# Kernel optimization log

Hardware: AMD Instinct MI355X
Metric: run time of the kernel (lower is better)

The kernel has to match this reference:

```python
import jax, jax.numpy as jnp
import numpy as np


def setup_inputs() -> dict:
    key = jax.random.key(0)
    ks = jax.random.split(key, 9)
    B, C, H, W = 8, 256, 64, 64
    Co = 256
    s = 1.0 / np.sqrt(C)
    return {
        "x": jax.random.normal(ks[0], (B, C, H, W), dtype=jnp.float32),
        "wq": jax.random.normal(ks[1], (Co, C), dtype=jnp.float32) * s,
        "bq": jnp.zeros((Co,), dtype=jnp.float32),
        "wk": jax.random.normal(ks[2], (Co, C), dtype=jnp.float32) * s,
        "bk": jnp.zeros((Co,), dtype=jnp.float32),
        "wv": jax.random.normal(ks[3], (Co, C), dtype=jnp.float32) * s,
        "bv": jnp.zeros((Co,), dtype=jnp.float32),
        "wo": jax.random.normal(ks[4], (C, Co), dtype=jnp.float32) * s,
        "bo": jnp.zeros((C,), dtype=jnp.float32),
    }


def reference(x, wq, bq, wk, bk, wv, bv, wo, bo):
    B, C, H, W = x.shape
    # 1x1 conv == per-pixel matmul. Flatten spatial dims: [B, N, C], N = H*W
    xf = x.reshape(B, C, H * W).transpose(0, 2, 1)  # [B, N, C]
    q = jnp.einsum("bnc,oc->bno", xf, wq) + bq      # [B, N, Co]
    k = jnp.einsum("bnc,oc->bno", xf, wk) + bk      # [B, N, Co]
    v = jnp.einsum("bnc,oc->bno", xf, wv) + bv      # [B, N, Co]
    # attention[b, i, j] = q[b, i] . k[b, j]  (no scaling, matches source)
    attn = jax.nn.softmax(jnp.einsum("bio,bjo->bij", q, k), axis=-1)  # [B, N, N]
    # out[b, i, c] = sum_j attn[b, i, j] * v[b, j, c]
    out = jnp.einsum("bij,bjo->bio", attn, v)       # [B, N, Co]
    out = jnp.einsum("bno,co->bnc", out, wo) + bo   # [B, N, C]
    return out.transpose(0, 2, 1).reshape(B, C, H, W)
```

## Files before the change

kernel.cpp:

```cpp
#include <hip/hip_runtime.h>
#include <hip/hip_fp16.h>

typedef _Float16 f16;
typedef _Float16 f16x4 __attribute__((ext_vector_type(4)));
typedef _Float16 f16x8 __attribute__((ext_vector_type(8)));
typedef float f32x4 __attribute__((ext_vector_type(4)));
typedef float f32x16 __attribute__((ext_vector_type(16)));
typedef unsigned int u32;
typedef u32 u32x4 __attribute__((ext_vector_type(4)));

static constexpr int CB = 8;
static constexpr int CC = 256;
static constexpr int CN = 4096;

#define MFMA(a, b, c)   __builtin_amdgcn_mfma_f32_16x16x32_f16((a), (b), (c), 0, 0, 0)
#define MFMA32(a, b, c) __builtin_amdgcn_mfma_f32_32x32x16_f16((a), (b), (c), 0, 0, 0)

__device__ __forceinline__ void gll16(const void* g, void* l) {
  __builtin_amdgcn_global_load_lds(
      (const __attribute__((address_space(1))) unsigned int*)g,
      (__attribute__((address_space(3))) unsigned int*)l, 16, 0, 0);
}

__device__ __forceinline__ void plswap(u32& a, u32& b) {
  asm volatile("v_permlane32_swap_b32 %0, %1" : "+v"(a), "+v"(b));
}

__device__ __forceinline__ u32 pk(float lo, float hi) {
  auto h = __builtin_amdgcn_cvt_pkrtz(lo, hi);
  return __builtin_bit_cast(u32, h);
}

__global__ __launch_bounds__(256) void prep_weights(const float* __restrict__ wq,
    const float* __restrict__ wk, const float* __restrict__ wv,
    const float* __restrict__ wo, f16* __restrict__ W) {
  int i = blockIdx.x * 256 + threadIdx.x;
  W[i]          = (f16)wq[i];
  W[65536 + i]  = (f16)wk[i];
  W[131072 + i] = (f16)wv[i];
  W[196608 + i] = (f16)wo[i];
}

__global__ __launch_bounds__(256) void qkv_kernel(const float* __restrict__ x,
    const f16* __restrict__ Wq, const f16* __restrict__ Wk, const f16* __restrict__ Wv,
    const float* __restrict__ bq, const float* __restrict__ bk, const float* __restrict__ bv,
    f16* __restrict__ Q, f16* __restrict__ K, f16* __restrict__ Vt) {
  __shared__ f16 xf[64][264];
  const int b  = blockIdx.x >> 6;
  const int n0 = (blockIdx.x & 63) << 6;
  const int t  = threadIdx.x;
  const float* xb = x + (size_t)b * CC * CN;
  {
    int c = t >> 4;
    const int nn = (t & 15) << 2;
    #pragma unroll
    for (int pass = 0; pass < 16; ++pass, c += 16) {
      const float4 v = *(const float4*)(xb + (size_t)c * CN + n0 + nn);
      xf[nn + 0][c] = (f16)v.x;
      xf[nn + 1][c] = (f16)v.y;
      xf[nn + 2][c] = (f16)v.z;
      xf[nn + 3][c] = (f16)v.w;
    }
  }
  __syncthreads();
  const int w = t >> 6, l = t & 63, lr = l & 15, lh = l >> 4;

  f16x8 xff[8];
  #pragma unroll
  for (int kk = 0; kk < 8; ++kk)
    xff[kk] = *(const f16x8*)&xf[w * 16 + lr][kk * 32 + lh * 8];

  const size_t qkrow = ((size_t)b * CN + n0 + w * 16 + lr) * CC;

  #pragma unroll 1
  for (int mat = 0; mat < 2; ++mat) {
    const f16* W = mat ? Wk : Wq;
    const float* bias = mat ? bk : bq;
    f16* dst = mat ? K : Q;
    f32x4 acc[16];
    #pragma unroll
    for (int m = 0; m < 16; ++m) acc[m] = f32x4{0.f, 0.f, 0.f, 0.f};
    #pragma unroll
    for (int kk = 0; kk < 8; ++kk) {
      #pragma unroll
      for (int m = 0; m < 16; ++m) {
        f16x8 af = *(const f16x8*)&W[(size_t)(m * 16 + lr) * CC + kk * 32 + lh * 8];
        acc[m] = MFMA(af, xff[kk], acc[m]);
      }
    }
    #pragma unroll
    for (int m = 0; m < 16; ++m) {
      const int o = m * 16 + lh * 4;
      const float4 bs = *(const float4*)&bias[o];
      f16x4 hv;
      hv[0] = (f16)(acc[m][0] + bs.x);
      hv[1] = (f16)(acc[m][1] + bs.y);
      hv[2] = (f16)(acc[m][2] + bs.z);
      hv[3] = (f16)(acc[m][3] + bs.w);
      *(f16x4*)&dst[qkrow + o] = hv;
    }
  }
  {
    f32x4 acc[16];
    #pragma unroll
    for (int m = 0; m < 16; ++m) acc[m] = f32x4{0.f, 0.f, 0.f, 0.f};
    #pragma unroll
    for (int kk = 0; kk < 8; ++kk) {
      #pragma unroll
      for (int m = 0; m < 16; ++m) {
        f16x8 bf = *(const f16x8*)&Wv[(size_t)(m * 16 + lr) * CC + kk * 32 + lh * 8];
        acc[m] = MFMA(xff[kk], bf, acc[m]);
      }
    }
    #pragma unroll
    for (int m = 0; m < 16; ++m) {
      const int o = m * 16 + lr;
      const float bvs = bv[o];
      f16x4 hv;
      #pragma unroll
      for (int j = 0; j < 4; ++j) hv[j] = (f16)(acc[m][j] + bvs);
      *(f16x4*)&Vt[((size_t)b * CC + o) * CN + n0 + w * 16 + lh * 4] = hv;
    }
  }
}

__global__ __launch_bounds__(256, 2) void attn_kernel(const f16* __restrict__ Q,
    const f16* __restrict__ K, const f16* __restrict__ Vt,
    const f16* __restrict__ Wo, const float* __restrict__ bo,
    float* __restrict__ out) {
  __shared__ __align__(16) char SMEM[75264];

  const int bid = blockIdx.x;
  const int lb = ((bid & 7) << 6) | (bid >> 3);
  const int b  = lb >> 6;
  const int q0 = (lb & 63) << 6;
  const int par = (bid >> 3) & 1;
  const int tid = threadIdx.x;
  const int w  = tid >> 6, l = tid & 63, ln = l & 31, lh = l >> 5;
  const int g  = w >> 1, hv = w & 1;

  const f16* Qb = Q  + (size_t)b * CN * CC;
  const f16* Kb = K  + (size_t)b * CN * CC;
  const f16* Vb = Vt + (size_t)b * CC * CN;

  auto kfrm = [&](int buf, int ks) -> char* { return SMEM + (buf << 14) + (ks << 10); };
  auto vfrm = [&](int buf, int f)  -> char* { return SMEM + 32768 + (buf << 14) + (f << 10); };
  auto pfrm = [&](int pb, int fr)  -> char* { return SMEM + 65536 + (pb << 12) + (g << 11) + (fr << 10); };
  float* const MLm = (float*)(SMEM + 73728 + g * 256);
  float* const MLl = MLm + 32;
  auto AFa = [&](int pb) -> float* { return (float*)(SMEM + 74240 + (pb << 9) + (g << 8)); };

  auto stageK = [&](int buf, int kv0) {
    const f16* ksrc = Kb + (size_t)(kv0 + ln) * CC + (w * 4) * 16 + 8 * lh;
    #pragma unroll
    for (int j = 0; j < 4; ++j)
      gll16(ksrc + j * 16, kfrm(buf, w * 4 + j));
  };
  auto stageV = [&](int buf, int kv0) {
    #pragma unroll
    for (int p = 0; p < 2; ++p) {
      const int f = w * 4 + 2 * p;
      const f16* vsrc = Vb + (size_t)((f >> 1) * 32 + ln) * CN + kv0 + 8 * lh;
      gll16(vsrc,      vfrm(buf, f));
      gll16(vsrc + 16, vfrm(buf, f + 1));
    }
  };

  const int qrow = q0 + 32 * g + ln;
  f16x8 qf[16];
  #pragma unroll
  for (int ks = 0; ks < 16; ++ks)
    qf[ks] = *(const f16x8*)(Qb + (size_t)qrow * CC + ks * 16 + 8 * lh);

  f32x16 oacc[4];
  #pragma unroll
  for (int ot = 0; ot < 4; ++ot)
    #pragma unroll
    for (int i = 0; i < 16; ++i) oacc[ot][i] = 0.0f;

  auto pvstep = [&](int pb) {
    const float* af = AFa(pb);
    const float flag = af[32];
    if (flag != 0.0f) {
      #pragma unroll
      for (int r = 0; r < 16; ++r) {
        const float fr = af[(r & 3) + 8 * (r >> 2) + 4 * lh];
        #pragma unroll
        for (int ot = 0; ot < 4; ++ot) oacc[ot][r] *= fr;
      }
    }
    const f16x8 pa0 = *(const f16x8*)(pfrm(pb, 0) + l * 16);
    const f16x8 pa1 = *(const f16x8*)(pfrm(pb, 1) + l * 16);
    __builtin_amdgcn_s_setprio(1);
    #pragma unroll
    for (int ot = 0; ot < 4; ++ot) {
      const int f0 = 8 * hv + 2 * ot;
      const f16x8 v0 = *(const f16x8*)(vfrm(pb, f0) + l * 16);
      oacc[ot] = MFMA32(pa0, v0, oacc[ot]);
      const f16x8 v1 = *(const f16x8*)(vfrm(pb, f0 + 1) + l * 16);
      oacc[ot] = MFMA32(pa1, v1, oacc[ot]);
    }
    __builtin_amdgcn_s_setprio(0);
  };

  stageK(0, 0);
  __syncthreads();

  #pragma unroll 1
  for (int it = 0; it < 128; ++it) {
    const int cur = it & 1, prv = cur ^ 1;
    if (it < 127) stageK(prv, (it + 1) * 32);
    stageV(cur, it * 32);

    const bool own = (hv == ((it + par) & 1));

    f32x16 s;
    if (own) {
      f32x16 sa, sb;
      #pragma unroll
      for (int i = 0; i < 16; ++i) { sa[i] = 0.0f; sb[i] = 0.0f; }
      __builtin_amdgcn_s_setprio(1);
      #pragma unroll
      for (int ks = 0; ks < 8; ++ks) {
        const f16x8 kf0 = *(const f16x8*)(kfrm(cur, ks) + l * 16);
        sa = MFMA32(kf0, qf[ks], sa);
        const f16x8 kf1 = *(const f16x8*)(kfrm(cur, ks + 8) + l * 16);
        sb = MFMA32(kf1, qf[ks + 8], sb);
      }
      __builtin_amdgcn_s_setprio(0);
      #pragma unroll
      for (int i = 0; i < 16; ++i) s[i] = sa[i] + sb[i];
    }

    if (it > 0) pvstep(prv);

    if (own) {
      const float mprev = it ? MLm[ln] : -3e38f;
      const float lprev = it ? MLl[ln] : 0.0f;
      float mx8[8], mx4[4];
      #pragma unroll
      for (int i = 0; i < 8; ++i) mx8[i] = fmaxf(s[2 * i], s[2 * i + 1]);
      #pragma unroll
      for (int i = 0; i < 4; ++i) mx4[i] = fmaxf(mx8[2 * i], mx8[2 * i + 1]);
      float pmax = fmaxf(fmaxf(mx4[0], mx4[1]), fmaxf(mx4[2], mx4[3]));
      pmax = fmaxf(pmax, __shfl_xor(pmax, 32));
      const bool need = !__all(pmax - mprev <= 8.0f);
      const float mnew = need ? fmaxf(mprev, pmax) : mprev;
      float p[16];
      #pragma unroll
      for (int r = 0; r < 16; ++r) p[r] = __expf(s[r] - mnew);
      float sm8[8], sm4[4];
      #pragma unroll
      for (int i = 0; i < 8; ++i) sm8[i] = p[2 * i] + p[2 * i + 1];
      #pragma unroll
      for (int i = 0; i < 4; ++i) sm4[i] = sm8[2 * i] + sm8[2 * i + 1];
      float psum = (sm4[0] + sm4[1]) + (sm4[2] + sm4[3]);
      psum += __shfl_xor(psum, 32);
      float alpha = 1.0f, lnew;
      if (need) { alpha = __expf(mprev - mnew); lnew = lprev * alpha + psum; }
      else      { lnew = lprev + psum; }
      if (l < 32) {
        MLm[ln] = mnew;
        MLl[ln] = lnew;
        float* af = AFa(cur);
        af[ln] = alpha;
        if (ln == 0) af[32] = need ? 1.0f : 0.0f;
      }
      u32 pw[8];
      #pragma unroll
      for (int i = 0; i < 8; ++i) pw[i] = pk(p[2 * i], p[2 * i + 1]);
      plswap(pw[0], pw[2]); plswap(pw[1], pw[3]);
      plswap(pw[4], pw[6]); plswap(pw[5], pw[7]);
      *(u32x4*)(pfrm(cur, 0) + l * 16) = u32x4{pw[0], pw[1], pw[2], pw[3]};
      *(u32x4*)(pfrm(cur, 1) + l * 16) = u32x4{pw[4], pw[5], pw[6], pw[7]};
    }
    __syncthreads();
  }

  pvstep(1);
  float invv[16];
  #pragma unroll
  for (int r = 0; r < 16; ++r)
    invv[r] = 1.0f / MLl[(r & 3) + 8 * (r >> 2) + 4 * lh];
  __syncthreads();

  f16* const OT = (f16*)SMEM;
  #pragma unroll
  for (int r = 0; r < 16; ++r) {
    const int q = (r & 3) + 8 * (r >> 2) + 4 * lh;
    const int qq = 32 * g + q;
    #pragma unroll
    for (int ot = 0; ot < 4; ++ot)
      OT[qq * 264 + 128 * hv + ot * 32 + ln] = (f16)(oacc[ot][r] * invv[r]);
  }
  __syncthreads();

  {
    const int lr = l & 15, lq = l >> 4;
    const f16* orow = OT + (w * 16 + lr) * 264;
    f32x4 acc[16];
    #pragma unroll
    for (int m = 0; m < 16; ++m) acc[m] = f32x4{0.f, 0.f, 0.f, 0.f};
    #pragma unroll
    for (int kk = 0; kk < 8; ++kk) {
      const f16x8 bf = *(const f16x8*)&orow[kk * 32 + lq * 8];
      #pragma unroll
      for (int m = 0; m < 16; ++m) {
        f16x8 af = *(const f16x8*)&Wo[(size_t)(m * 16 + lr) * CC + kk * 32 + lq * 8];
        acc[m] = MFMA(af, bf, acc[m]);
      }
    }
    #pragma unroll
    for (int m = 0; m < 16; ++m) {
      const int c = m * 16 + lq * 4;
      const float4 bv4 = *(const float4*)&bo[c];
      const size_t base = ((size_t)b * CC + c) * CN + q0 + w * 16 + lr;
      out[base + 0 * (size_t)CN] = acc[m][0] + bv4.x;
      out[base + 1 * (size_t)CN] = acc[m][1] + bv4.y;
      out[base + 2 * (size_t)CN] = acc[m][2] + bv4.z;
      out[base + 3 * (size_t)CN] = acc[m][3] + bv4.w;
    }
  }
}

extern "C" void kernel_launch(void* const* d_in, const int* in_sizes, int n_in,
                              void* d_out, int out_size, void* d_ws, size_t ws_size,
                              hipStream_t stream) {
  const float* x  = (const float*)d_in[0];
  const float* wq = (const float*)d_in[1];
  const float* bq = (const float*)d_in[2];
  const float* wk = (const float*)d_in[3];
  const float* bk = (const float*)d_in[4];
  const float* wv = (const float*)d_in[5];
  const float* bv = (const float*)d_in[6];
  const float* wo = (const float*)d_in[7];
  const float* bo = (const float*)d_in[8];

  f16* W  = (f16*)d_ws;
  f16* Qd = W + 262144;
  f16* Kd = Qd + (size_t)CB * CN * CC;
  f16* Vt = Kd + (size_t)CB * CN * CC;

  prep_weights<<<256, 256, 0, stream>>>(wq, wk, wv, wo, W);
  qkv_kernel<<<512, 256, 0, stream>>>(x, W, W + 65536, W + 131072, bq, bk, bv, Qd, Kd, Vt);
  attn_kernel<<<512, 256, 0, stream>>>(Qd, Kd, Vt, W + 196608, bo, (float*)d_out);
}
```

Measured before the change: 378.2 us.

## Switch QKV projection to 32x32 MFMA tiles with 2 waves per block

Restructures the QKV projection kernel to use 128-thread blocks where each wave handles 32 pixels with 32x32x16 MFMAs instead of 16x16x32, processing two 32-wide output tiles at a time. Each weight fragment loaded from global memory now feeds a larger MFMA, cutting weight-load traffic per unit of work and the total instruction count. In exchange there are fewer waves per block (less latency hiding during the x staging loads), more registers are held in the x fragment array, and each thread does twice as many staging passes.

```diff
diff --git a/kernel.cpp b/kernel.cpp
--- a/kernel.cpp
+++ b/kernel.cpp
@@ -41,7 +41,7 @@
   W[196608 + i] = (f16)wo[i];
 }
 
-__global__ __launch_bounds__(256) void qkv_kernel(const float* __restrict__ x,
+__global__ __launch_bounds__(128) void qkv_kernel(const float* __restrict__ x,
     const f16* __restrict__ Wq, const f16* __restrict__ Wk, const f16* __restrict__ Wv,
     const float* __restrict__ bq, const float* __restrict__ bk, const float* __restrict__ bv,
     f16* __restrict__ Q, f16* __restrict__ K, f16* __restrict__ Vt) {
@@ -54,7 +54,7 @@
     int c = t >> 4;
     const int nn = (t & 15) << 2;
     #pragma unroll
-    for (int pass = 0; pass < 16; ++pass, c += 16) {
+    for (int pass = 0; pass < 32; ++pass, c += 8) {
       const float4 v = *(const float4*)(xb + (size_t)c * CN + n0 + nn);
       xf[nn + 0][c] = (f16)v.x;
       xf[nn + 1][c] = (f16)v.y;
@@ -63,63 +63,79 @@
     }
   }
   __syncthreads();
-  const int w = t >> 6, l = t & 63, lr = l & 15, lh = l >> 4;
-
-  f16x8 xff[8];
-  #pragma unroll
-  for (int kk = 0; kk < 8; ++kk)
-    xff[kk] = *(const f16x8*)&xf[w * 16 + lr][kk * 32 + lh * 8];
-
-  const size_t qkrow = ((size_t)b * CN + n0 + w * 16 + lr) * CC;
+  const int w = t >> 6, l = t & 63, ln = l & 31, lh = l >> 5;
+
+  f16x8 xff[16];
+  #pragma unroll
+  for (int kt = 0; kt < 16; ++kt)
+    xff[kt] = *(const f16x8*)&xf[w * 32 + ln][kt * 16 + lh * 8];
+
+  const size_t qkrow = ((size_t)b * CN + n0 + w * 32 + ln) * CC;
 
   #pragma unroll 1
   for (int mat = 0; mat < 2; ++mat) {
     const f16* W = mat ? Wk : Wq;
     const float* bias = mat ? bk : bq;
     f16* dst = mat ? K : Q;
-    f32x4 acc[16];
-    #pragma unroll
-    for (int m = 0; m < 16; ++m) acc[m] = f32x4{0.f, 0.f, 0.f, 0.f};
-    #pragma unroll
-    for (int kk = 0; kk < 8; ++kk) {
-      #pragma unroll
-      for (int m = 0; m < 16; ++m) {
-        f16x8 af = *(const f16x8*)&W[(size_t)(m * 16 + lr) * CC + kk * 32 + lh * 8];
-        acc[m] = MFMA(af, xff[kk], acc[m]);
-      }
-    }
-    #pragma unroll
-    for (int m = 0; m < 16; ++m) {
-      const int o = m * 16 + lh * 4;
-      const float4 bs = *(const float4*)&bias[o];
-      f16x4 hv;
-      hv[0] = (f16)(acc[m][0] + bs.x);
-      hv[1] = (f16)(acc[m][1] + bs.y);
-      hv[2] = (f16)(acc[m][2] + bs.z);
-      hv[3] = (f16)(acc[m][3] + bs.w);
-      *(f16x4*)&dst[qkrow + o] = hv;
-    }
-  }
-  {
-    f32x4 acc[16];
-    #pragma unroll
-    for (int m = 0; m < 16; ++m) acc[m] = f32x4{0.f, 0.f, 0.f, 0.f};
-    #pragma unroll
-    for (int kk = 0; kk < 8; ++kk) {
-      #pragma unroll
-      for (int m = 0; m < 16; ++m) {
-        f16x8 bf = *(const f16x8*)&Wv[(size_t)(m * 16 + lr) * CC + kk * 32 + lh * 8];
-        acc[m] = MFMA(xff[kk], bf, acc[m]);
-      }
-    }
-    #pragma unroll
-    for (int m = 0; m < 16; ++m) {
-      const int o = m * 16 + lr;
-      const float bvs = bv[o];
-      f16x4 hv;
-      #pragma unroll
-      for (int j = 0; j < 4; ++j) hv[j] = (f16)(acc[m][j] + bvs);
-      *(f16x4*)&Vt[((size_t)b * CC + o) * CN + n0 + w * 16 + lh * 4] = hv;
+    #pragma unroll 1
+    for (int ot = 0; ot < 8; ot += 2) {
+      f32x16 a0, a1;
+      #pragma unroll
+      for (int i = 0; i < 16; ++i) { a0[i] = 0.0f; a1[i] = 0.0f; }
+      #pragma unroll
+      for (int kt = 0; kt < 16; ++kt) {
+        const f16x8 af0 = *(const f16x8*)&W[(size_t)(ot * 32 + ln) * CC + kt * 16 + lh * 8];
+        a0 = MFMA32(af0, xff[kt], a0);
+        const f16x8 af1 = *(const f16x8*)&W[(size_t)(ot * 32 + 32 + ln) * CC + kt * 16 + lh * 8];
+        a1 = MFMA32(af1, xff[kt], a1);
+      }
+      #pragma unroll
+      for (int rg = 0; rg < 4; ++rg) {
+        const int o = ot * 32 + rg * 8 + lh * 4;
+        const float4 b0 = *(const float4*)&bias[o];
+        const float4 b1 = *(const float4*)&bias[o + 32];
+        f16x4 h0, h1;
+        h0[0] = (f16)(a0[rg * 4 + 0] + b0.x);
+        h0[1] = (f16)(a0[rg * 4 + 1] + b0.y);
+        h0[2] = (f16)(a0[rg * 4 + 2] + b0.z);
+        h0[3] = (f16)(a0[rg * 4 + 3] + b0.w);
+        h1[0] = (f16)(a1[rg * 4 + 0] + b1.x);
+        h1[1] = (f16)(a1[rg * 4 + 1] + b1.y);
+        h1[2] = (f16)(a1[rg * 4 + 2] + b1.z);
+        h1[3] = (f16)(a1[rg * 4 + 3] + b1.w);
+        *(f16x4*)&dst[qkrow + o]      = h0;
+        *(f16x4*)&dst[qkrow + o + 32] = h1;
+      }
+    }
+  }
+
+  #pragma unroll 1
+  for (int ot = 0; ot < 8; ot += 2) {
+    f32x16 a0, a1;
+    #pragma unroll
+    for (int i = 0; i < 16; ++i) { a0[i] = 0.0f; a1[i] = 0.0f; }
+    #pragma unroll
+    for (int kt = 0; kt < 16; ++kt) {
+      const f16x8 wf0 = *(const f16x8*)&Wv[(size_t)(ot * 32 + ln) * CC + kt * 16 + lh * 8];
+      a0 = MFMA32(xff[kt], wf0, a0);
+      const f16x8 wf1 = *(const f16x8*)&Wv[(size_t)(ot * 32 + 32 + ln) * CC + kt * 16 + lh * 8];
+      a1 = MFMA32(xff[kt], wf1, a1);
+    }
+    const int o0 = ot * 32 + ln, o1 = o0 + 32;
+    const float bv0 = bv[o0], bv1 = bv[o1];
+    f16* v0 = &Vt[((size_t)b * CC + o0) * CN + n0 + w * 32];
+    f16* v1 = &Vt[((size_t)b * CC + o1) * CN + n0 + w * 32];
+    #pragma unroll
+    for (int rg = 0; rg < 4; ++rg) {
+      const int nn = rg * 8 + lh * 4;
+      f16x4 h0, h1;
+      #pragma unroll
+      for (int j = 0; j < 4; ++j) {
+        h0[j] = (f16)(a0[rg * 4 + j] + bv0);
+        h1[j] = (f16)(a1[rg * 4 + j] + bv1);
+      }
+      *(f16x4*)&v0[nn] = h0;
+      *(f16x4*)&v1[nn] = h1;
     }
   }
 }
@@ -342,6 +358,6 @@
   f16* Vt = Kd + (size_t)CB * CN * CC;
 
   prep_weights<<<256, 256, 0, stream>>>(wq, wk, wv, wo, W);
-  qkv_kernel<<<512, 256, 0, stream>>>(x, W, W + 65536, W + 131072, bq, bk, bv, Qd, Kd, Vt);
+  qkv_kernel<<<512, 128, 0, stream>>>(x, W, W + 65536, W + 131072, bq, bk, bv, Qd, Kd, Vt);
   attn_kernel<<<512, 256, 0, stream>>>(Qd, Kd, Vt, W + 196608, bo, (float*)d_out);
 }
```

Result: faster. 336.7 us (-11.0%).
